# Optimization experiments

Hardware: AMD Instinct MI355X
Metric: run time of the kernel (lower is better)

Reference implementation:

```python
import jax, jax.numpy as jnp
import numpy as np

B, T, D, H, L = 2, 1024, 1024, 16, 4
HD = D // H            # head_dim = 64
DFF = 4096             # 4 * d_model
VOCAB = 16384          # max_vocab_size (tied head)
MAX_CHAR = 8192        # max_char_len for RoPE table
EPS = 1e-6


def setup_inputs() -> dict:
    key = jax.random.key(0)
    ks = jax.random.split(key, 12)
    s = 0.02
    return {
        "token_ids": jax.random.randint(ks[0], (B, T), 0, 259, dtype=jnp.int32),
        "position_ids": jnp.sort(jax.random.randint(ks[1], (B, T), 0, MAX_CHAR, dtype=jnp.int32), axis=-1),
        "embed": jax.random.normal(ks[2], (VOCAB, D), jnp.float32) * s,
        "attn_norm_w": jnp.ones((L, D), jnp.float32),
        "wq": jax.random.normal(ks[3], (L, D, D), jnp.float32) * s,
        "wk": jax.random.normal(ks[4], (L, D, D), jnp.float32) * s,
        "wv": jax.random.normal(ks[5], (L, D, D), jnp.float32) * s,
        "wo": jax.random.normal(ks[6], (L, D, D), jnp.float32) * s,
        "ff_norm_w": jnp.ones((L, D), jnp.float32),
        "w1": jax.random.normal(ks[7], (L, DFF, D), jnp.float32) * s,
        "w2": jax.random.normal(ks[8], (L, D, DFF), jnp.float32) * s,
        "w3": jax.random.normal(ks[9], (L, DFF, D), jnp.float32) * s,
        "norm_w": jnp.ones((D,), jnp.float32),
    }


def _rmsnorm(x, w):
    return x * jax.lax.rsqrt(jnp.mean(x * x, axis=-1, keepdims=True) + EPS) * w


def _rope_tables():
    # precompute_freqs_cis: angles[t, i] = t / theta^(2i/dim)
    inv = 1.0 / (10000.0 ** (jnp.arange(0, HD, 2, dtype=jnp.float32) / HD))  # [HD/2]
    ang = jnp.arange(MAX_CHAR, dtype=jnp.float32)[:, None] * inv[None, :]    # [MAX_CHAR, HD/2]
    return jnp.cos(ang), jnp.sin(ang)


def _apply_rope(x, cos, sin):
    # x: [B,T,H,HD]; cos/sin: [B,T,1,HD/2] (complex multiply on (even,odd) pairs)
    xp = x.reshape(B, T, H, HD // 2, 2)
    xr, xi = xp[..., 0], xp[..., 1]
    out = jnp.stack([xr * cos - xi * sin, xr * sin + xi * cos], axis=-1)
    return out.reshape(B, T, H, HD)


def reference(token_ids, position_ids, embed, attn_norm_w, wq, wk, wv, wo,
              ff_norm_w, w1, w2, w3, norm_w):
    cos_tab, sin_tab = _rope_tables()
    cos = cos_tab[position_ids][:, :, None, :]  # [B,T,1,HD/2]
    sin = sin_tab[position_ids][:, :, None, :]

    x = embed[token_ids]  # [B,T,D] (no ghost tokens active)
    scale = 1.0 / np.sqrt(HD)

    for l in range(L):
        # --- attention block ---
        h = _rmsnorm(x, attn_norm_w[l])
        q = jnp.einsum('btd,od->bto', h, wq[l]).reshape(B, T, H, HD)
        k = jnp.einsum('btd,od->bto', h, wk[l]).reshape(B, T, H, HD)
        v = jnp.einsum('btd,od->bto', h, wv[l]).reshape(B, T, H, HD)
        q = _apply_rope(q, cos, sin)
        k = _apply_rope(k, cos, sin)
        attn = jnp.einsum('bthd,bshd->bhts', q, k) * scale  # no mask in model forward
        attn = jax.nn.softmax(attn, axis=-1)
        o = jnp.einsum('bhts,bshd->bthd', attn, v).reshape(B, T, D)
        x = x + jnp.einsum('btd,od->bto', o, wo[l])
        # --- SwiGLU FFN ---
        h = _rmsnorm(x, ff_norm_w[l])
        g = jax.nn.silu(jnp.einsum('btd,fd->btf', h, w1[l])) * jnp.einsum('btd,fd->btf', h, w3[l])
        x = x + jnp.einsum('btf,df->btd', g, w2[l])

    x = _rmsnorm(x, norm_w)
    return jnp.einsum('btd,vd->btv', x, embed)  # tied LM head -> [B,T,VOCAB]
```

## Files before the change

### kernel.cpp

```cpp
#include <hip/hip_runtime.h>

#define NTOK 2048
#define DMODEL 1024
#define NHEADS 16
#define HD_ 64
#define TSEQ 1024
#define DFF_ 4096
#define NVOCAB 16384

typedef unsigned short u16;
typedef unsigned int u32;
typedef __bf16 bf16x8 __attribute__((ext_vector_type(8)));
typedef float floatx4 __attribute__((ext_vector_type(4)));

__device__ __forceinline__ u16 f2bf(float f) {
  u32 u = __float_as_uint(f);
  u += 0x7FFFu + ((u >> 16) & 1u);
  return (u16)(u >> 16);
}
__device__ __forceinline__ float bf2f(u16 h) {
  return __uint_as_float(((u32)h) << 16);
}

__device__ __forceinline__ void gload_lds16(const void* g, void* l) {
  __builtin_amdgcn_global_load_lds(
      (const __attribute__((address_space(1))) void*)g,
      (__attribute__((address_space(3))) void*)l, 16, 0, 0);
}

__global__ void convert_bf16(const float* __restrict__ src, u16* __restrict__ dst, int n4) {
  int i = blockIdx.x * blockDim.x + threadIdx.x;
  int stride = gridDim.x * blockDim.x;
  for (; i < n4; i += stride) {
    float4 v = ((const float4*)src)[i];
    ushort4 o;
    o.x = f2bf(v.x); o.y = f2bf(v.y); o.z = f2bf(v.z); o.w = f2bf(v.w);
    ((ushort4*)dst)[i] = o;
  }
}

__global__ void convert_layer(const float* __restrict__ wq, const float* __restrict__ wk,
                              const float* __restrict__ wv, const float* __restrict__ wo,
                              const float* __restrict__ w1, const float* __restrict__ w3,
                              const float* __restrict__ w2,
                              u16* __restrict__ wqkv, u16* __restrict__ wo_b,
                              u16* __restrict__ w13, u16* __restrict__ w2_b) {
  int i = blockIdx.x * blockDim.x + threadIdx.x;
  int stride = gridDim.x * blockDim.x;
  for (; i < 4194304; i += stride) {
    const float* s; u16* d; int j;
    if (i < 262144)       { s = wq; d = wqkv;           j = i; }
    else if (i < 524288)  { s = wk; d = wqkv + 1048576; j = i - 262144; }
    else if (i < 786432)  { s = wv; d = wqkv + 2097152; j = i - 524288; }
    else if (i < 1048576) { s = wo; d = wo_b;           j = i - 786432; }
    else if (i < 2097152) { s = w1; d = w13;            j = i - 1048576; }
    else if (i < 3145728) { s = w3; d = w13 + 4194304;  j = i - 2097152; }
    else                  { s = w2; d = w2_b;           j = i - 3145728; }
    float4 v = ((const float4*)s)[j];
    ushort4 o;
    o.x = f2bf(v.x); o.y = f2bf(v.y); o.z = f2bf(v.z); o.w = f2bf(v.w);
    ((ushort4*)d)[j] = o;
  }
}

__global__ void gather_embed(const int* __restrict__ tok, const float* __restrict__ embed,
                             float* __restrict__ x) {
  int m = blockIdx.x;
  int t = tok[m];
  float4 v = ((const float4*)(embed + (long)t * DMODEL))[threadIdx.x];
  ((float4*)(x + (long)m * DMODEL))[threadIdx.x] = v;
}

__global__ void rmsnorm_bf16(const float* __restrict__ x, const float* __restrict__ w,
                             u16* __restrict__ out) {
  __shared__ float red[9];
  int m = blockIdx.x;
  int tid = threadIdx.x, lane = tid & 63, wave = tid >> 6;
  float4 v = ((const float4*)(x + (long)m * DMODEL))[tid];
  float ss = v.x * v.x + v.y * v.y + v.z * v.z + v.w * v.w;
  for (int o2 = 32; o2 > 0; o2 >>= 1) ss += __shfl_down(ss, o2);
  if (lane == 0) red[wave] = ss;
  __syncthreads();
  if (tid == 0) red[8] = rsqrtf((red[0] + red[1] + red[2] + red[3]) * (1.0f / 1024.0f) + 1e-6f);
  __syncthreads();
  float inv = red[8];
  float4 wv = ((const float4*)w)[tid];
  ushort4 o;
  o.x = f2bf(v.x * inv * wv.x); o.y = f2bf(v.y * inv * wv.y);
  o.z = f2bf(v.z * inv * wv.z); o.w = f2bf(v.w * inv * wv.w);
  ((ushort4*)(out + (long)m * DMODEL))[tid] = o;
}

__global__ void rope_qk(u16* __restrict__ qkv, const int* __restrict__ pos_ids) {
  __shared__ float cs[32], sn[32];
  int m = blockIdx.x;
  int tid = threadIdx.x;
  if (tid < 32) {
    float inv = expf(-(float)tid * (9.210340371976184f / 32.0f));
    float ang = (float)pos_ids[m] * inv;
    float s, c;
    sincosf(ang, &s, &c);
    cs[tid] = c; sn[tid] = s;
  }
  __syncthreads();
  u16* row = qkv + (long)m * 3072;
  for (int part = 0; part < 2; part++) {
    u16* base = row + part * 1024;
    for (int pp = tid; pp < 512; pp += 256) {
      int i = pp & 31;
      u32* p = (u32*)(base + pp * 2);
      u32 v = *p;
      float xr = bf2f((u16)(v & 0xFFFF));
      float xi = bf2f((u16)(v >> 16));
      float c = cs[i], s = sn[i];
      float orr = xr * c - xi * s;
      float oii = xr * s + xi * c;
      *p = (u32)f2bf(orr) | ((u32)f2bf(oii) << 16);
    }
  }
}

__global__ void transpose_v(const u16* __restrict__ qkv, u16* __restrict__ vT) {
  __shared__ u16 tile[64][65];
  int tb = blockIdx.x;
  int bh = blockIdx.y;
  int b = bh >> 4, h = bh & 15;
  const u16* src = qkv + ((long)(b * TSEQ + tb * 64)) * 3072 + 2048 + h * 64;
  for (int i = 0; i < 16; i++) {
    int e = threadIdx.x + i * 256;
    int t = e >> 6, d = e & 63;
    tile[t][d] = src[(long)t * 3072 + d];
  }
  __syncthreads();
  u16* dst = vT + ((long)bh * 64) * TSEQ + tb * 64;
  for (int i = 0; i < 16; i++) {
    int e = threadIdx.x + i * 256;
    int d = e >> 6, t = e & 63;
    dst[(long)d * TSEQ + t] = tile[t][d];
  }
}

__global__ void softmax_rows(u16* __restrict__ S) {
  __shared__ float red[9];
  long row = blockIdx.x;
  u16* p = S + row * 1024;
  int tid = threadIdx.x, lane = tid & 63, wave = tid >> 6;
  ushort4 v4 = ((const ushort4*)p)[tid];
  float v0 = bf2f(v4.x), v1 = bf2f(v4.y), v2 = bf2f(v4.z), v3 = bf2f(v4.w);
  float mx = fmaxf(fmaxf(v0, v1), fmaxf(v2, v3));
  for (int o2 = 32; o2 > 0; o2 >>= 1) mx = fmaxf(mx, __shfl_down(mx, o2));
  if (lane == 0) red[wave] = mx;
  __syncthreads();
  if (tid == 0) red[8] = fmaxf(fmaxf(red[0], red[1]), fmaxf(red[2], red[3]));
  __syncthreads();
  mx = red[8];
  float e0 = __expf(v0 - mx), e1 = __expf(v1 - mx), e2 = __expf(v2 - mx), e3 = __expf(v3 - mx);
  float s = e0 + e1 + e2 + e3;
  for (int o2 = 32; o2 > 0; o2 >>= 1) s += __shfl_down(s, o2);
  if (lane == 0) red[wave] = s;
  __syncthreads();
  if (tid == 0) red[8] = red[0] + red[1] + red[2] + red[3];
  __syncthreads();
  float inv = 1.0f / red[8];
  ushort4 o;
  o.x = f2bf(e0 * inv); o.y = f2bf(e1 * inv); o.z = f2bf(e2 * inv); o.w = f2bf(e3 * inv);
  ((ushort4*)p)[tid] = o;
}

__global__ void swiglu(const u16* __restrict__ t13, u16* __restrict__ g) {
  int i = blockIdx.x * 256 + threadIdx.x;
  int m = i >> 9, f8 = i & 511;
  const ushort4* pa = (const ushort4*)(t13 + (long)m * 8192 + f8 * 8);
  const ushort4* pb = (const ushort4*)(t13 + (long)m * 8192 + 4096 + f8 * 8);
  ushort4 a0 = pa[0], a1 = pa[1];
  ushort4 b0 = pb[0], b1 = pb[1];
  ushort4 o0, o1;
  float a, b;
#define SWG(av, bv, ov) \
  a = bf2f(av); b = bf2f(bv); ov = f2bf(a * b / (1.0f + __expf(-a)));
  SWG(a0.x, b0.x, o0.x) SWG(a0.y, b0.y, o0.y) SWG(a0.z, b0.z, o0.z) SWG(a0.w, b0.w, o0.w)
  SWG(a1.x, b1.x, o1.x) SWG(a1.y, b1.y, o1.y) SWG(a1.z, b1.z, o1.z) SWG(a1.w, b1.w, o1.w)
#undef SWG
  ushort4* po = (ushort4*)(g + (long)m * 4096 + f8 * 8);
  po[0] = o0; po[1] = o1;
}

template <int BM, int BN, int WR, int WC>
__global__ __launch_bounds__(WR * WC * 64) void gemm_nt(
    const u16* __restrict__ A, int lda, long a_sb, long a_sh,
    const u16* __restrict__ B, int ldb, long b_sb, long b_sh,
    void* __restrict__ C, int ldc, long c_sb, long c_sh,
    int K, float scale, int mode) {
  constexpr int NW = WR * WC;
  constexpr int NTHR = NW * 64;
  constexpr int WTM = BM / WR;
  constexpr int WTN = BN / WC;
  constexpr int MT = WTM / 16;
  constexpr int NT = WTN / 16;
  constexpr int ISA = (BM * 64) / (NTHR * 16);
  constexpr int ISB = (BN * 64) / (NTHR * 16);
  static_assert(ISA >= 1 && ISB >= 1, "tile too small");

  __shared__ __align__(16) u16 lA[BM * 32];
  __shared__ __align__(16) u16 lB[BN * 32];

  const int tid = threadIdx.x;
  const int lane = tid & 63;
  const int wave = tid >> 6;
  const int wm = wave / WC;
  const int wn = wave % WC;
  const int m0 = blockIdx.y * BM;
  const int n0 = blockIdx.x * BN;
  const int zb = blockIdx.z >> 4;
  const int zh = blockIdx.z & 15;
  A += (long)zb * a_sb + (long)zh * a_sh;
  B += (long)zb * b_sb + (long)zh * b_sh;
  const long c0 = (long)zb * c_sb + (long)zh * c_sh;

  floatx4 acc[MT][NT];
  for (int mi = 0; mi < MT; mi++)
    for (int ni = 0; ni < NT; ni++)
      for (int r = 0; r < 4; r++) acc[mi][ni][r] = 0.0f;

  const int q_ = lane >> 4;

  for (int k0 = 0; k0 < K; k0 += 32) {
    const u16* Ag = A + (long)m0 * lda + k0;
#pragma unroll
    for (int i = 0; i < ISA; i++) {
      int e = (tid + i * NTHR) * 8;
      int r = e >> 5;
      int c = (e >> 3) & 3;
      int csw = c ^ ((r >> 1) & 3);
      gload_lds16(Ag + (long)r * lda + (csw << 3), &lA[e]);
    }
    const u16* Bg = B + (long)n0 * ldb + k0;
#pragma unroll
    for (int i = 0; i < ISB; i++) {
      int e = (tid + i * NTHR) * 8;
      int r = e >> 5;
      int c = (e >> 3) & 3;
      int csw = c ^ ((r >> 1) & 3);
      gload_lds16(Bg + (long)r * ldb + (csw << 3), &lB[e]);
    }
    __syncthreads();

    bf16x8 af[MT], bfr[NT];
#pragma unroll
    for (int mi = 0; mi < MT; mi++) {
      int r = wm * WTM + mi * 16 + (lane & 15);
      af[mi] = *(const bf16x8*)&lA[(r << 5) + ((q_ ^ ((r >> 1) & 3)) << 3)];
    }
#pragma unroll
    for (int ni = 0; ni < NT; ni++) {
      int r = wn * WTN + ni * 16 + (lane & 15);
      bfr[ni] = *(const bf16x8*)&lB[(r << 5) + ((q_ ^ ((r >> 1) & 3)) << 3)];
    }
#pragma unroll
    for (int mi = 0; mi < MT; mi++)
#pragma unroll
      for (int ni = 0; ni < NT; ni++)
        acc[mi][ni] = __builtin_amdgcn_mfma_f32_16x16x32_bf16(af[mi], bfr[ni], acc[mi][ni], 0, 0, 0);
    __syncthreads();
  }

#pragma unroll
  for (int mi = 0; mi < MT; mi++) {
#pragma unroll
    for (int ni = 0; ni < NT; ni++) {
      int col = n0 + wn * WTN + ni * 16 + (lane & 15);
      int rbase = m0 + wm * WTM + mi * 16 + (lane >> 4) * 4;
#pragma unroll
      for (int r = 0; r < 4; r++) {
        float v = acc[mi][ni][r] * scale;
        long idx = c0 + (long)(rbase + r) * ldc + col;
        if (mode == 0)       ((float*)C)[idx] = v;
        else if (mode == 1)  ((u16*)C)[idx] = f2bf(v);
        else                 ((float*)C)[idx] += v;
      }
    }
  }
}

template <int MODE>
__global__ __launch_bounds__(512, 2) void gemm256_nt(
    const u16* __restrict__ A, int lda,
    const u16* __restrict__ B, int ldb,
    void* __restrict__ C, int ldc,
    int K, float scale) {
  __shared__ __align__(16) u16 lA[2][16384];
  __shared__ __align__(16) u16 lB[2][16384];

  const int tid = threadIdx.x;
  const int lane = tid & 63;
  const int wave = tid >> 6;
  const int wm = wave >> 2;
  const int wn = wave & 3;
  const int m0 = blockIdx.y * 256;
  const int n0 = blockIdx.x * 256;
  const int q = lane >> 4;
  const int rl = lane & 15;

  const int ck0 = ((q ^ (rl & 7)) << 3);
  const int ck1 = (((4 | q) ^ (rl & 7)) << 3);
  const int aRow = wm * 128 + rl;
  const int bRow = wn * 64 + rl;

  int sr[4], sc[4];
#pragma unroll
  for (int i = 0; i < 4; i++) {
    int s = tid + i * 512;
    sr[i] = s >> 3;
    sc[i] = (((s & 7) ^ ((s >> 3) & 7)) << 3);
  }

#define STAGE256(k0, buf)                                                      \
  {                                                                            \
    _Pragma("unroll")                                                          \
    for (int i = 0; i < 4; i++)                                                \
      gload_lds16(A + (long)(m0 + sr[i]) * lda + (k0) + sc[i],                 \
                  &lA[buf][(tid + i * 512) * 8]);                              \
    _Pragma("unroll")                                                          \
    for (int i = 0; i < 4; i++)                                                \
      gload_lds16(B + (long)(n0 + sr[i]) * ldb + (k0) + sc[i],                 \
                  &lB[buf][(tid + i * 512) * 8]);                              \
  }

  floatx4 acc[8][4];
#pragma unroll
  for (int mi = 0; mi < 8; mi++)
#pragma unroll
    for (int ni = 0; ni < 4; ni++)
#pragma unroll
      for (int r = 0; r < 4; r++) acc[mi][ni][r] = 0.0f;

  const int NKT = K >> 6;
  STAGE256(0, 0);
  if (NKT > 1) {
    STAGE256(64, 1);
    asm volatile("s_waitcnt vmcnt(8)" ::: "memory");
  } else {
    asm volatile("s_waitcnt vmcnt(0)" ::: "memory");
  }
  __builtin_amdgcn_s_barrier();
  __builtin_amdgcn_sched_barrier(0);

  int cur = 0;
  for (int t = 0; t < NKT; t++) {
    const u16* pA = &lA[cur][0];
    const u16* pB = &lB[cur][0];
    bf16x8 aF[4][2], b01[2][2], b23[2][2];

#pragma unroll
    for (int mi = 0; mi < 4; mi++) {
      aF[mi][0] = *(const bf16x8*)&pA[(aRow + mi * 16) * 64 + ck0];
      aF[mi][1] = *(const bf16x8*)&pA[(aRow + mi * 16) * 64 + ck1];
    }
#pragma unroll
    for (int ni = 0; ni < 2; ni++) {
      b01[ni][0] = *(const bf16x8*)&pB[(bRow + ni * 16) * 64 + ck0];
      b01[ni][1] = *(const bf16x8*)&pB[(bRow + ni * 16) * 64 + ck1];
    }
    __builtin_amdgcn_s_setprio(1);
#pragma unroll
    for (int mi = 0; mi < 4; mi++)
#pragma unroll
      for (int ni = 0; ni < 2; ni++) {
        acc[mi][ni] = __builtin_amdgcn_mfma_f32_16x16x32_bf16(aF[mi][0], b01[ni][0], acc[mi][ni], 0, 0, 0);
        acc[mi][ni] = __builtin_amdgcn_mfma_f32_16x16x32_bf16(aF[mi][1], b01[ni][1], acc[mi][ni], 0, 0, 0);
      }
    __builtin_amdgcn_s_setprio(0);

#pragma unroll
    for (int ni = 0; ni < 2; ni++) {
      b23[ni][0] = *(const bf16x8*)&pB[(bRow + (ni + 2) * 16) * 64 + ck0];
      b23[ni][1] = *(const bf16x8*)&pB[(bRow + (ni + 2) * 16) * 64 + ck1];
    }
    __builtin_amdgcn_s_setprio(1);
#pragma unroll
    for (int mi = 0; mi < 4; mi++)
#pragma unroll
      for (int ni = 0; ni < 2; ni++) {
        acc[mi][ni + 2] = __builtin_amdgcn_mfma_f32_16x16x32_bf16(aF[mi][0], b23[ni][0], acc[mi][ni + 2], 0, 0, 0);
        acc[mi][ni + 2] = __builtin_amdgcn_mfma_f32_16x16x32_bf16(aF[mi][1], b23[ni][1], acc[mi][ni + 2], 0, 0, 0);
      }
    __builtin_amdgcn_s_setprio(0);

#pragma unroll
    for (int mi = 0; mi < 4; mi++) {
      aF[mi][0] = *(const bf16x8*)&pA[(aRow + (mi + 4) * 16) * 64 + ck0];
      aF[mi][1] = *(const bf16x8*)&pA[(aRow + (mi + 4) * 16) * 64 + ck1];
    }
    __builtin_amdgcn_s_setprio(1);
#pragma unroll
    for (int mi = 0; mi < 4; mi++)
#pragma unroll
      for (int ni = 0; ni < 2; ni++) {
        acc[mi + 4][ni + 2] = __builtin_amdgcn_mfma_f32_16x16x32_bf16(aF[mi][0], b23[ni][0], acc[mi + 4][ni + 2], 0, 0, 0);
        acc[mi + 4][ni + 2] = __builtin_amdgcn_mfma_f32_16x16x32_bf16(aF[mi][1], b23[ni][1], acc[mi + 4][ni + 2], 0, 0, 0);
      }
    __builtin_amdgcn_s_setprio(0);
    asm volatile("s_waitcnt lgkmcnt(0)" ::: "memory");
    __builtin_amdgcn_s_barrier();
    __builtin_amdgcn_sched_barrier(0);

    if (t + 2 < NKT) STAGE256((t + 2) << 6, cur);
    __builtin_amdgcn_s_setprio(1);
#pragma unroll
    for (int mi = 0; mi < 4; mi++)
#pragma unroll
      for (int ni = 0; ni < 2; ni++) {
        acc[mi + 4][ni] = __builtin_amdgcn_mfma_f32_16x16x32_bf16(aF[mi][0], b01[ni][0], acc[mi + 4][ni], 0, 0, 0);
        acc[mi + 4][ni] = __builtin_amdgcn_mfma_f32_16x16x32_bf16(aF[mi][1], b01[ni][1], acc[mi + 4][ni], 0, 0, 0);
      }
    __builtin_amdgcn_s_setprio(0);
    if (t + 1 < NKT) {
      if (t + 2 < NKT) asm volatile("s_waitcnt vmcnt(8)" ::: "memory");
      else             asm volatile("s_waitcnt vmcnt(0)" ::: "memory");
      __builtin_amdgcn_s_barrier();
      __builtin_amdgcn_sched_barrier(0);
    }
    cur ^= 1;
  }
#undef STAGE256

#pragma unroll
  for (int mi = 0; mi < 8; mi++) {
    int row = m0 + wm * 128 + mi * 16 + q * 4;
#pragma unroll
    for (int ni = 0; ni < 4; ni++) {
      int col = n0 + wn * 64 + ni * 16 + rl;
#pragma unroll
      for (int r = 0; r < 4; r++) {
        float v = acc[mi][ni][r] * scale;
        long idx = (long)(row + r) * ldc + col;
        if (MODE == 0) ((float*)C)[idx] = v;
        else           ((u16*)C)[idx] = f2bf(v);
      }
    }
  }
}

extern "C" void kernel_launch(void* const* d_in, const int* in_sizes, int n_in,
                              void* d_out, int out_size, void* d_ws, size_t ws_size,
                              hipStream_t stream) {
  const int*   tok         = (const int*)d_in[0];
  const int*   pos         = (const int*)d_in[1];
  const float* embed       = (const float*)d_in[2];
  const float* attn_norm_w = (const float*)d_in[3];
  const float* wq          = (const float*)d_in[4];
  const float* wk          = (const float*)d_in[5];
  const float* wv          = (const float*)d_in[6];
  const float* wo          = (const float*)d_in[7];
  const float* ff_norm_w   = (const float*)d_in[8];
  const float* w1          = (const float*)d_in[9];
  const float* w2          = (const float*)d_in[10];
  const float* w3          = (const float*)d_in[11];
  const float* norm_w      = (const float*)d_in[12];

  char* ws = (char*)d_ws;
  u16*   ebf  = (u16*)(ws);
  u16*   wqkv = (u16*)(ws + 33554432);
  u16*   wo_b = (u16*)(ws + 39845888);
  u16*   w13  = (u16*)(ws + 41943040);
  u16*   w2_b = (u16*)(ws + 58720256);
  float* x    = (float*)(ws + 67108864);
  u16*   h    = (u16*)(ws + 75497472);
  u16*   qkv  = (u16*)(ws + 79691776);
  u16*   vT   = (u16*)(ws + 92274688);
  u16*   o    = (u16*)(ws + 96468992);
  u16*   S    = (u16*)(ws + 100663296);
  u16*   t13  = S;
  u16*   g    = (u16*)(ws + 134217728);

  convert_bf16<<<16384, 256, 0, stream>>>(embed, ebf, NVOCAB * DMODEL / 4);
  gather_embed<<<NTOK, 256, 0, stream>>>(tok, embed, x);

  for (int l = 0; l < 4; l++) {
    convert_layer<<<16384, 256, 0, stream>>>(
        wq + (long)l * 1048576, wk + (long)l * 1048576, wv + (long)l * 1048576,
        wo + (long)l * 1048576, w1 + (long)l * 4194304, w3 + (long)l * 4194304,
        w2 + (long)l * 4194304, wqkv, wo_b, w13, w2_b);

    rmsnorm_bf16<<<NTOK, 256, 0, stream>>>(x, attn_norm_w + l * 1024, h);
    gemm_nt<128, 128, 2, 2><<<dim3(24, 16, 1), 256, 0, stream>>>(
        h, 1024, 0, 0, wqkv, 1024, 0, 0, qkv, 3072, 0, 0, 1024, 1.0f, 1);
    rope_qk<<<NTOK, 256, 0, stream>>>(qkv, pos);
    transpose_v<<<dim3(16, 32), 256, 0, stream>>>(qkv, vT);
    gemm_nt<128, 128, 2, 2><<<dim3(8, 8, 32), 256, 0, stream>>>(
        qkv, 3072, 3145728L, 64L,
        qkv + 1024, 3072, 3145728L, 64L,
        S, 1024, 16777216L, 1048576L, 64, 0.125f, 1);
    softmax_rows<<<32768, 256, 0, stream>>>(S);
    gemm_nt<64, 64, 2, 2><<<dim3(1, 16, 32), 256, 0, stream>>>(
        S, 1024, 16777216L, 1048576L,
        vT, 1024, 1048576L, 65536L,
        o, 1024, 1048576L, 64L, 1024, 1.0f, 1);
    gemm_nt<64, 128, 2, 2><<<dim3(8, 32, 1), 256, 0, stream>>>(
        o, 1024, 0, 0, wo_b, 1024, 0, 0, x, 1024, 0, 0, 1024, 1.0f, 2);

    rmsnorm_bf16<<<NTOK, 256, 0, stream>>>(x, ff_norm_w + l * 1024, h);
    gemm256_nt<1><<<dim3(32, 8, 1), 512, 0, stream>>>(
        h, 1024, w13, 1024, t13, 8192, 1024, 1.0f);
    swiglu<<<4096, 256, 0, stream>>>(t13, g);
    gemm_nt<64, 128, 2, 2><<<dim3(8, 32, 1), 256, 0, stream>>>(
        g, 4096, 0, 0, w2_b, 4096, 0, 0, x, 1024, 0, 0, 4096, 1.0f, 2);
  }

  rmsnorm_bf16<<<NTOK, 256, 0, stream>>>(x, norm_w, h);
  gemm256_nt<0><<<dim3(64, 8, 1), 512, 0, stream>>>(
      h, 1024, ebf, 1024, d_out, 16384, 1024, 1.0f);
}
```

Baseline: 1.523 ms.

## Split 256x256 GEMM staging into half-tile loads interleaved with MFMA phases

Reworks the 256x256 NT GEMM main loop so global-to-LDS staging is issued as four half-tile loads, each placed between MFMA quadrants, instead of one bulk stage after the first barrier. It also changes the per-wave output mapping to interleaved 64/32-row halves, and adds an XCD-aware block-id remap that groups consecutive workgroups onto the same chiplet for L2 reuse. The aim is to spread memory traffic across the iteration and hide load latency behind compute. In exchange it adds several extra barriers per K-step, and the finer-grained waitcnt accounting is more fragile.

```diff
diff --git a/kernel.cpp b/kernel.cpp
--- a/kernel.cpp
+++ b/kernel.cpp
@@ -296,35 +296,45 @@
   const int wave = tid >> 6;
   const int wm = wave >> 2;
   const int wn = wave & 3;
-  const int m0 = blockIdx.y * 256;
-  const int n0 = blockIdx.x * 256;
+
+  int bid = blockIdx.y * gridDim.x + blockIdx.x;
+  const int nwg = gridDim.x * gridDim.y;
+  if ((nwg & 7) == 0) bid = (bid & 7) * (nwg >> 3) + (bid >> 3);
+  const int m0 = (bid / gridDim.x) * 256;
+  const int n0 = (bid % gridDim.x) * 256;
+
   const int q = lane >> 4;
   const int rl = lane & 15;
-
   const int ck0 = ((q ^ (rl & 7)) << 3);
   const int ck1 = (((4 | q) ^ (rl & 7)) << 3);
-  const int aRow = wm * 128 + rl;
-  const int bRow = wn * 64 + rl;
-
-  int sr[4], sc[4];
-#pragma unroll
-  for (int i = 0; i < 4; i++) {
-    int s = tid + i * 512;
-    sr[i] = s >> 3;
-    sc[i] = (((s & 7) ^ ((s >> 3) & 7)) << 3);
-  }
-
-#define STAGE256(k0, buf)                                                      \
+  const int aLo = (wm * 64 + rl) * 64;
+  const int aHi = (128 + wm * 64 + rl) * 64;
+  const int bLo = (wn * 32 + rl) * 64;
+  const int bHi = (128 + wn * 32 + rl) * 64;
+
+  const int s0 = tid, s1 = tid + 512;
+  const int sr0 = s0 >> 3, sr1 = s1 >> 3;
+  const int sc0 = ((s0 & 7) ^ (sr0 & 7)) << 3;
+  const int sc1 = ((s1 & 7) ^ (sr1 & 7)) << 3;
+
+#define STAGEH(gbase, ld, ldsbase)                                             \
   {                                                                            \
+    const u16* g_ = (gbase);                                                   \
+    u16* d_ = (ldsbase);                                                       \
+    gload_lds16(g_ + (long)sr0 * (ld) + sc0, d_ + s0 * 8);                     \
+    gload_lds16(g_ + (long)sr1 * (ld) + sc1, d_ + s1 * 8);                     \
+  }
+
+#define MFMAQ(RO, CO, AF, BF)                                                  \
+  _Pragma("unroll")                                                            \
+  for (int mi = 0; mi < 4; mi++)                                               \
     _Pragma("unroll")                                                          \
-    for (int i = 0; i < 4; i++)                                                \
-      gload_lds16(A + (long)(m0 + sr[i]) * lda + (k0) + sc[i],                 \
-                  &lA[buf][(tid + i * 512) * 8]);                              \
-    _Pragma("unroll")                                                          \
-    for (int i = 0; i < 4; i++)                                                \
-      gload_lds16(B + (long)(n0 + sr[i]) * ldb + (k0) + sc[i],                 \
-                  &lB[buf][(tid + i * 512) * 8]);                              \
-  }
+    for (int ni = 0; ni < 2; ni++) {                                           \
+      acc[mi + RO][ni + CO] = __builtin_amdgcn_mfma_f32_16x16x32_bf16(         \
+          AF[mi][0], BF[ni][0], acc[mi + RO][ni + CO], 0, 0, 0);               \
+      acc[mi + RO][ni + CO] = __builtin_amdgcn_mfma_f32_16x16x32_bf16(         \
+          AF[mi][1], BF[ni][1], acc[mi + RO][ni + CO], 0, 0, 0);               \
+    }
 
   floatx4 acc[8][4];
 #pragma unroll
@@ -335,101 +345,99 @@
       for (int r = 0; r < 4; r++) acc[mi][ni][r] = 0.0f;
 
   const int NKT = K >> 6;
-  STAGE256(0, 0);
+
+  STAGEH(A + (long)m0 * lda, lda, &lA[0][0]);
+  STAGEH(A + (long)(m0 + 128) * lda, lda, &lA[0][8192]);
+  STAGEH(B + (long)n0 * ldb, ldb, &lB[0][0]);
+  STAGEH(B + (long)(n0 + 128) * ldb, ldb, &lB[0][8192]);
   if (NKT > 1) {
-    STAGE256(64, 1);
-    asm volatile("s_waitcnt vmcnt(8)" ::: "memory");
+    STAGEH(A + (long)m0 * lda + 64, lda, &lA[1][0]);
+    STAGEH(B + (long)n0 * ldb + 64, ldb, &lB[1][0]);
+    STAGEH(B + (long)(n0 + 128) * ldb + 64, ldb, &lB[1][8192]);
+    asm volatile("s_waitcnt vmcnt(6)" ::: "memory");
   } else {
     asm volatile("s_waitcnt vmcnt(0)" ::: "memory");
   }
   __builtin_amdgcn_s_barrier();
-  __builtin_amdgcn_sched_barrier(0);
-
-  int cur = 0;
+
+  bf16x8 aF[4][2], b01[2][2], b23[2][2];
+
+#pragma unroll 2
   for (int t = 0; t < NKT; t++) {
-    const u16* pA = &lA[cur][0];
-    const u16* pB = &lB[cur][0];
-    bf16x8 aF[4][2], b01[2][2], b23[2][2];
+    const int buf = t & 1;
+    const u16* pA = lA[buf];
+    const u16* pB = lB[buf];
 
 #pragma unroll
     for (int mi = 0; mi < 4; mi++) {
-      aF[mi][0] = *(const bf16x8*)&pA[(aRow + mi * 16) * 64 + ck0];
-      aF[mi][1] = *(const bf16x8*)&pA[(aRow + mi * 16) * 64 + ck1];
+      aF[mi][0] = *(const bf16x8*)&pA[aLo + mi * 1024 + ck0];
+      aF[mi][1] = *(const bf16x8*)&pA[aLo + mi * 1024 + ck1];
     }
 #pragma unroll
     for (int ni = 0; ni < 2; ni++) {
-      b01[ni][0] = *(const bf16x8*)&pB[(bRow + ni * 16) * 64 + ck0];
-      b01[ni][1] = *(const bf16x8*)&pB[(bRow + ni * 16) * 64 + ck1];
-    }
+      b01[ni][0] = *(const bf16x8*)&pB[bLo + ni * 1024 + ck0];
+      b01[ni][1] = *(const bf16x8*)&pB[bLo + ni * 1024 + ck1];
+    }
+    if (t + 1 < NKT)
+      STAGEH(A + (long)(m0 + 128) * lda + (t + 1) * 64, lda, &lA[buf ^ 1][8192]);
+    asm volatile("s_waitcnt lgkmcnt(8)" ::: "memory");
+    __builtin_amdgcn_s_barrier();
+    asm volatile("s_waitcnt lgkmcnt(0)" ::: "memory");
     __builtin_amdgcn_s_setprio(1);
-#pragma unroll
-    for (int mi = 0; mi < 4; mi++)
-#pragma unroll
-      for (int ni = 0; ni < 2; ni++) {
-        acc[mi][ni] = __builtin_amdgcn_mfma_f32_16x16x32_bf16(aF[mi][0], b01[ni][0], acc[mi][ni], 0, 0, 0);
-        acc[mi][ni] = __builtin_amdgcn_mfma_f32_16x16x32_bf16(aF[mi][1], b01[ni][1], acc[mi][ni], 0, 0, 0);
-      }
+    MFMAQ(0, 0, aF, b01)
     __builtin_amdgcn_s_setprio(0);
+    __builtin_amdgcn_s_barrier();
 
 #pragma unroll
     for (int ni = 0; ni < 2; ni++) {
-      b23[ni][0] = *(const bf16x8*)&pB[(bRow + (ni + 2) * 16) * 64 + ck0];
-      b23[ni][1] = *(const bf16x8*)&pB[(bRow + (ni + 2) * 16) * 64 + ck1];
-    }
+      b23[ni][0] = *(const bf16x8*)&pB[bHi + ni * 1024 + ck0];
+      b23[ni][1] = *(const bf16x8*)&pB[bHi + ni * 1024 + ck1];
+    }
+    if (t + 2 < NKT)
+      STAGEH(A + (long)m0 * lda + (t + 2) * 64, lda, &lA[buf][0]);
+    __builtin_amdgcn_s_barrier();
+    asm volatile("s_waitcnt lgkmcnt(0)" ::: "memory");
     __builtin_amdgcn_s_setprio(1);
-#pragma unroll
-    for (int mi = 0; mi < 4; mi++)
-#pragma unroll
-      for (int ni = 0; ni < 2; ni++) {
-        acc[mi][ni + 2] = __builtin_amdgcn_mfma_f32_16x16x32_bf16(aF[mi][0], b23[ni][0], acc[mi][ni + 2], 0, 0, 0);
-        acc[mi][ni + 2] = __builtin_amdgcn_mfma_f32_16x16x32_bf16(aF[mi][1], b23[ni][1], acc[mi][ni + 2], 0, 0, 0);
-      }
+    MFMAQ(0, 2, aF, b23)
     __builtin_amdgcn_s_setprio(0);
+    __builtin_amdgcn_s_barrier();
 
 #pragma unroll
     for (int mi = 0; mi < 4; mi++) {
-      aF[mi][0] = *(const bf16x8*)&pA[(aRow + (mi + 4) * 16) * 64 + ck0];
-      aF[mi][1] = *(const bf16x8*)&pA[(aRow + (mi + 4) * 16) * 64 + ck1];
-    }
+      aF[mi][0] = *(const bf16x8*)&pA[aHi + mi * 1024 + ck0];
+      aF[mi][1] = *(const bf16x8*)&pA[aHi + mi * 1024 + ck1];
+    }
+    if (t + 2 < NKT)
+      STAGEH(B + (long)n0 * ldb + (t + 2) * 64, ldb, &lB[buf][0]);
+    __builtin_amdgcn_s_barrier();
+    asm volatile("s_waitcnt lgkmcnt(0)" ::: "memory");
     __builtin_amdgcn_s_setprio(1);
-#pragma unroll
-    for (int mi = 0; mi < 4; mi++)
-#pragma unroll
-      for (int ni = 0; ni < 2; ni++) {
-        acc[mi + 4][ni + 2] = __builtin_amdgcn_mfma_f32_16x16x32_bf16(aF[mi][0], b23[ni][0], acc[mi + 4][ni + 2], 0, 0, 0);
-        acc[mi + 4][ni + 2] = __builtin_amdgcn_mfma_f32_16x16x32_bf16(aF[mi][1], b23[ni][1], acc[mi + 4][ni + 2], 0, 0, 0);
-      }
+    MFMAQ(4, 2, aF, b23)
     __builtin_amdgcn_s_setprio(0);
-    asm volatile("s_waitcnt lgkmcnt(0)" ::: "memory");
     __builtin_amdgcn_s_barrier();
-    __builtin_amdgcn_sched_barrier(0);
-
-    if (t + 2 < NKT) STAGE256((t + 2) << 6, cur);
+
+    if (t + 2 < NKT)
+      STAGEH(B + (long)(n0 + 128) * ldb + (t + 2) * 64, ldb, &lB[buf][8192]);
     __builtin_amdgcn_s_setprio(1);
-#pragma unroll
-    for (int mi = 0; mi < 4; mi++)
-#pragma unroll
-      for (int ni = 0; ni < 2; ni++) {
-        acc[mi + 4][ni] = __builtin_amdgcn_mfma_f32_16x16x32_bf16(aF[mi][0], b01[ni][0], acc[mi + 4][ni], 0, 0, 0);
-        acc[mi + 4][ni] = __builtin_amdgcn_mfma_f32_16x16x32_bf16(aF[mi][1], b01[ni][1], acc[mi + 4][ni], 0, 0, 0);
-      }
+    MFMAQ(4, 0, aF, b01)
     __builtin_amdgcn_s_setprio(0);
     if (t + 1 < NKT) {
-      if (t + 2 < NKT) asm volatile("s_waitcnt vmcnt(8)" ::: "memory");
+      if (t + 2 < NKT) asm volatile("s_waitcnt vmcnt(6)" ::: "memory");
       else             asm volatile("s_waitcnt vmcnt(0)" ::: "memory");
       __builtin_amdgcn_s_barrier();
-      __builtin_amdgcn_sched_barrier(0);
-    }
-    cur ^= 1;
-  }
-#undef STAGE256
+    }
+  }
+#undef STAGEH
+#undef MFMAQ
 
 #pragma unroll
   for (int mi = 0; mi < 8; mi++) {
-    int row = m0 + wm * 128 + mi * 16 + q * 4;
+    int rowBlk = (mi < 4) ? (wm * 64 + mi * 16) : (128 + wm * 64 + (mi - 4) * 16);
+    int row = m0 + rowBlk + q * 4;
 #pragma unroll
     for (int ni = 0; ni < 4; ni++) {
-      int col = n0 + wn * 64 + ni * 16 + rl;
+      int colBlk = (ni < 2) ? (wn * 32 + ni * 16) : (128 + wn * 32 + (ni - 2) * 16);
+      int col = n0 + colBlk + rl;
 #pragma unroll
       for (int r = 0; r < 4; r++) {
         float v = acc[mi][ni][r] * scale;
```

After: 1.545 ms. About the same (+1.5%).
